# Kernel optimization log

Hardware: AMD Instinct MI355X
Metric: run time of the kernel (lower is better)

## Reference

```python
import jax, jax.numpy as jnp
import numpy as np

EPS = 1e-08


def setup_inputs() -> dict:
    key = jax.random.key(0)
    k1, k2, k3, k4 = jax.random.split(key, 4)
    b, c, h, hw = 16, 512, 32, 32
    out_ch, kk, w_dim = 512, 3, 512
    fan_in = c * kk * kk
    return {
        "x": jax.random.normal(k1, (b, c, h, hw), dtype=jnp.float32),
        "w": jax.random.normal(k2, (b, w_dim), dtype=jnp.float32),
        "weight": jax.random.normal(k3, (out_ch, c, kk, kk), dtype=jnp.float32) / np.sqrt(fan_in),
        "affine_w": jax.random.normal(k4, (c, w_dim), dtype=jnp.float32) * 0.01,
        "affine_b": jnp.ones((c,), dtype=jnp.float32),
    }


def _modconv(x, w, weight, affine_w, affine_b, demod=True):
    b, c, h, hw = x.shape
    kk = weight.shape[-1]
    # style affine: (b, in_ch)
    style = w @ affine_w.T + affine_b
    # per-sample modulated weights: (b, out_ch, in_ch, k, k)
    wgt = weight[None] * style[:, None, :, None, None]
    if demod:
        d = jax.lax.rsqrt(jnp.sum(wgt ** 2, axis=(2, 3, 4)) + EPS)  # (b, out_ch)
        wgt = wgt * d[:, :, None, None, None]

    def conv_one(xi, wi):
        # xi: (c, h, w), wi: (out_ch, c, k, k)
        return jax.lax.conv_general_dilated(
            xi[None], wi, window_strides=(1, 1), padding="SAME",
            dimension_numbers=("NCHW", "OIHW", "NCHW"))[0]

    return jax.vmap(conv_one)(x, wgt)  # (b, out_ch, h, w)


def reference(x, w, weight, affine_w, affine_b):
    return _modconv(x, w, weight, affine_w, affine_b, demod=True)
```

## Files before the change

kernel.cpp:

```cpp
#include <hip/hip_runtime.h>


typedef __attribute__((ext_vector_type(8))) short bfx8;
typedef __attribute__((ext_vector_type(4))) float f32x4;
typedef __attribute__((ext_vector_type(4))) unsigned short us4;
typedef __attribute__((ext_vector_type(8))) unsigned short us8;

__device__ __forceinline__ unsigned short f2bf(float f) {
    unsigned int u = __builtin_bit_cast(unsigned int, f);
    u += 0x7FFFu + ((u >> 16) & 1u);
    return (unsigned short)(u >> 16);
}

__device__ __forceinline__ void gload_lds16(const void* g, void* l) {
    __builtin_amdgcn_global_load_lds(
        (const __attribute__((address_space(1))) unsigned int*)g,
        (__attribute__((address_space(3))) unsigned int*)l,
        16, 0, 0);
}

__device__ __forceinline__ float wave_sum(float v) {
    #pragma unroll
    for (int m = 1; m < 64; m <<= 1) v += __shfl_xor(v, m, 64);
    return v;
}

__device__ __forceinline__ int shift_of(int t) {
    const int tap = t >> 3, q = t & 7;
    const int ky = tap / 3, kx = tap - ky * 3;
    return (ky * 34 + kx) * 512 + q * 64;
}


__global__ void style_kernel(const float* __restrict__ w,
                             const float* __restrict__ affine_w,
                             const float* __restrict__ affine_b,
                             float* __restrict__ style) {
    const int out = blockIdx.x * 4 + (threadIdx.x >> 6);
    const int lane = threadIdx.x & 63;
    const int b = out >> 9, c = out & 511;
    const float4 a0 = *(const float4*)(affine_w + (size_t)c * 512 + lane * 8);
    const float4 a1 = *(const float4*)(affine_w + (size_t)c * 512 + lane * 8 + 4);
    const float4 w0 = *(const float4*)(w + (size_t)b * 512 + lane * 8);
    const float4 w1 = *(const float4*)(w + (size_t)b * 512 + lane * 8 + 4);
    float acc = a0.x * w0.x + a0.y * w0.y + a0.z * w0.z + a0.w * w0.w
              + a1.x * w1.x + a1.y * w1.y + a1.z * w1.z + a1.w * w1.w;
    acc = wave_sum(acc);
    if (lane == 0) style[out] = acc + affine_b[c];
}

__global__ void w2wbf_kernel(const float* __restrict__ weight,
                             float* __restrict__ W2,
                             unsigned short* __restrict__ wbf) {
    const int idx = blockIdx.x * 256 + threadIdx.x;
    const int oc = idx >> 9, c = idx & 511;
    const int q = c >> 6, c_local = c & 63;
    const int s = c_local >> 3, j = c_local & 7;
    const int pos = ((s ^ (oc & 7)) << 3) | j;
    const float* p = weight + (size_t)idx * 9;
    float ss = 0.f;
    #pragma unroll
    for (int t = 0; t < 9; ++t) {
        const float v = p[t];
        ss += v * v;
        wbf[((size_t)(t * 8 + q) * 512 + oc) * 64 + pos] = f2bf(v);
    }
    W2[idx] = ss;
}

__global__ void d_kernel(const float* __restrict__ style,
                         const float* __restrict__ W2,
                         float* __restrict__ dcoef) {
    const int out = blockIdx.x * 4 + (threadIdx.x >> 6);
    const int lane = threadIdx.x & 63;
    const int b = out >> 9, o = out & 511;
    const float4 s0 = *(const float4*)(style + (size_t)b * 512 + lane * 8);
    const float4 s1 = *(const float4*)(style + (size_t)b * 512 + lane * 8 + 4);
    const float4 v0 = *(const float4*)(W2 + (size_t)o * 512 + lane * 8);
    const float4 v1 = *(const float4*)(W2 + (size_t)o * 512 + lane * 8 + 4);
    float acc = s0.x * s0.x * v0.x + s0.y * s0.y * v0.y
              + s0.z * s0.z * v0.z + s0.w * s0.w * v0.w
              + s1.x * s1.x * v1.x + s1.y * s1.y * v1.y
              + s1.z * s1.z * v1.z + s1.w * s1.w * v1.w;
    acc = wave_sum(acc);
    if (lane == 0) dcoef[out] = rsqrtf(acc + 1e-8f);
}

__global__ void border_kernel(unsigned short* __restrict__ xs) {
    const int idx = blockIdx.x * 256 + threadIdx.x;
    const int b = idx / (132 * 128);
    const int r_ = idx - b * (132 * 128);
    const int cell = r_ >> 7, t = r_ & 127;
    int rr, cc;
    if (cell < 34)      { rr = 0;  cc = cell; }
    else if (cell < 68) { rr = 33; cc = cell - 34; }
    else { const int jj = cell - 68; rr = 1 + (jj >> 1); cc = (jj & 1) ? 33 : 0; }
    us4 z = (us4){0, 0, 0, 0};
    *(us4*)(xs + (((size_t)b * 34 + rr) * 34 + cc) * 512 + t * 4) = z;
}

__global__ void xspad_kernel(const float* __restrict__ x,
                             const float* __restrict__ style,
                             unsigned short* __restrict__ xs) {
    __shared__ __align__(16) unsigned short tile[128][36];
    const int b = blockIdx.z, h = blockIdx.y, c0 = blockIdx.x * 128;
    const int tid = threadIdx.x;
    #pragma unroll
    for (int it = 0; it < 4; ++it) {
        const int e = it * 256 + tid;
        const int ch = e >> 3, w4 = e & 7;
        const float4 v = *(const float4*)(x + (((size_t)b * 512 + c0 + ch) * 32 + h) * 32 + w4 * 4);
        const float sv = style[b * 512 + c0 + ch];
        us4 o;
        o.x = f2bf(v.x * sv); o.y = f2bf(v.y * sv);
        o.z = f2bf(v.z * sv); o.w = f2bf(v.w * sv);
        *(us4*)&tile[ch][w4 * 4] = o;
    }
    __syncthreads();
    #pragma unroll
    for (int it = 0; it < 2; ++it) {
        const int e = it * 256 + tid;
        const int cq = e & 15, w_ = e >> 4;
        us8 o;
        #pragma unroll
        for (int i = 0; i < 8; ++i) o[i] = tile[cq * 8 + i][w_];
        *(us8*)(xs + (((size_t)b * 34 + (h + 1)) * 34 + (w_ + 1)) * 512 + c0 + cq * 8) = o;
    }
}

#define LDS_RD(off) (*(const bfx8*)(lds + (off)))
#define MFMA(a, bb, c) __builtin_amdgcn_mfma_f32_16x16x32_bf16((a), (bb), (c), 0, 0, 0)

__global__ __launch_bounds__(512, 2) void conv_kernel(
    const unsigned short* __restrict__ wbf,
    const unsigned short* __restrict__ xs,
    const float* __restrict__ dcoef,
    float* __restrict__ out) {
    __shared__ __align__(16) char lds[147456];

    const int id = blockIdx.x;
    const int b = id >> 4;
    const int oc0 = ((id >> 2) & 3) << 7;
    const int n0  = (id & 3) << 8;

    const int tid = threadIdx.x;
    const int lane = tid & 63;
    const int wv = tid >> 6;
    const int wr = wv >> 2, wc = wv & 3;
    const int l7 = lane & 7, l15 = lane & 15;

    const int swz0 = ((lane >> 4) ^ l7) << 4;
    const int swz1 = (((lane >> 4) + 4) ^ l7) << 4;
    const int arow = (wr * 64 + l15) * 128;
    const int brow = 16384 + (wc * 64 + l15) * 128;

    const int lsub = lane >> 3;
    const int sx = l7 ^ lsub;
    const int ra0 = wv * 16 + lsub, ra1 = ra0 + 8;
    const int aoff0 = (oc0 + ra0) * 64 + l7 * 8;
    const int aoff1 = (oc0 + ra1) * 64 + l7 * 8;
    const int adst0 = (wv * 2) * 1024, adst1 = adst0 + 1024;
    size_t bbase[4]; int bdst[4];
    const size_t xsb = (size_t)b * (34 * 34 * 512);
    #pragma unroll
    for (int i = 0; i < 4; ++i) {
        const int p = wv * 32 + i * 8 + lsub;
        const int n = n0 + p;
        bbase[i] = xsb + ((size_t)(n >> 5) * 34 + (n & 31)) * 512 + sx * 8;
        bdst[i] = 16384 + (wv * 4 + i) * 1024;
    }

#define STAGE_A(tt, bo) do { \
        const unsigned short* wsrc_ = wbf + (size_t)(tt) * 32768; \
        gload_lds16(wsrc_ + aoff0, lds + (bo) + adst0); \
        gload_lds16(wsrc_ + aoff1, lds + (bo) + adst1); } while (0)
#define STAGE_B01(sh, bo) do { \
        gload_lds16(xs + bbase[0] + (sh), lds + (bo) + bdst[0]); \
        gload_lds16(xs + bbase[1] + (sh), lds + (bo) + bdst[1]); } while (0)
#define STAGE_B23(sh, bo) do { \
        gload_lds16(xs + bbase[2] + (sh), lds + (bo) + bdst[2]); \
        gload_lds16(xs + bbase[3] + (sh), lds + (bo) + bdst[3]); } while (0)
#define BARRIER() __builtin_amdgcn_s_barrier()
#define LGKM0() asm volatile("s_waitcnt lgkmcnt(0)" ::: "memory")

    f32x4 acc[4][4];
    #pragma unroll
    for (int i = 0; i < 4; ++i)
        #pragma unroll
        for (int j = 0; j < 4; ++j) acc[i][j] = (f32x4){0.f, 0.f, 0.f, 0.f};

    STAGE_A(0, 0);      STAGE_B01(0, 0);       STAGE_B23(0, 0);
    STAGE_A(1, 49152);  STAGE_B01(64, 49152);  STAGE_B23(64, 49152);
    asm volatile("s_waitcnt vmcnt(6)" ::: "memory");
    BARRIER();

    int co = 0;
    for (int t = 0; t < 72; ++t) {
        int so = co + 98304; if (so >= 147456) so -= 147456;
        const bool pf = (t < 70);
        const int sh2 = pf ? shift_of(t + 2) : 0;

        bfx8 a0[4], a1[4], b0, b1, b2, b3;

        #pragma unroll
        for (int mi = 0; mi < 4; ++mi) a0[mi] = LDS_RD(co + arow + mi * 2048 + swz0);
        b0 = LDS_RD(co + brow + 0 * 2048 + swz0);
        b1 = LDS_RD(co + brow + 1 * 2048 + swz0);
        if (pf) STAGE_A(t + 2, so);
        BARRIER(); LGKM0();
        __builtin_amdgcn_s_setprio(1);
        #pragma unroll
        for (int mi = 0; mi < 4; ++mi) acc[mi][0] = MFMA(a0[mi], b0, acc[mi][0]);
        #pragma unroll
        for (int mi = 0; mi < 4; ++mi) acc[mi][1] = MFMA(a0[mi], b1, acc[mi][1]);
        __builtin_amdgcn_s_setprio(0);
        BARRIER();

        b2 = LDS_RD(co + brow + 2 * 2048 + swz0);
        b3 = LDS_RD(co + brow + 3 * 2048 + swz0);
        if (pf) STAGE_B01(sh2, so);
        BARRIER(); LGKM0();
        __builtin_amdgcn_s_setprio(1);
        #pragma unroll
        for (int mi = 0; mi < 4; ++mi) acc[mi][2] = MFMA(a0[mi], b2, acc[mi][2]);
        #pragma unroll
        for (int mi = 0; mi < 4; ++mi) acc[mi][3] = MFMA(a0[mi], b3, acc[mi][3]);
        __builtin_amdgcn_s_setprio(0);
        BARRIER();

        #pragma unroll
        for (int mi = 0; mi < 4; ++mi) a1[mi] = LDS_RD(co + arow + mi * 2048 + swz1);
        b0 = LDS_RD(co + brow + 0 * 2048 + swz1);
        b1 = LDS_RD(co + brow + 1 * 2048 + swz1);
        if (pf) STAGE_B23(sh2, so);
        BARRIER(); LGKM0();
        __builtin_amdgcn_s_setprio(1);
        #pragma unroll
        for (int mi = 0; mi < 4; ++mi) acc[mi][0] = MFMA(a1[mi], b0, acc[mi][0]);
        #pragma unroll
        for (int mi = 0; mi < 4; ++mi) acc[mi][1] = MFMA(a1[mi], b1, acc[mi][1]);
        __builtin_amdgcn_s_setprio(0);
        BARRIER();

        b2 = LDS_RD(co + brow + 2 * 2048 + swz1);
        b3 = LDS_RD(co + brow + 3 * 2048 + swz1);
        BARRIER(); LGKM0();
        __builtin_amdgcn_s_setprio(1);
        #pragma unroll
        for (int mi = 0; mi < 4; ++mi) acc[mi][2] = MFMA(a1[mi], b2, acc[mi][2]);
        #pragma unroll
        for (int mi = 0; mi < 4; ++mi) acc[mi][3] = MFMA(a1[mi], b3, acc[mi][3]);
        __builtin_amdgcn_s_setprio(0);
        if (t < 70) { asm volatile("s_waitcnt vmcnt(6)" ::: "memory"); }
        else        { asm volatile("s_waitcnt vmcnt(0)" ::: "memory"); }
        BARRIER();

        co += 49152; if (co >= 147456) co -= 147456;
    }

    const int r4 = (lane >> 4) * 4;
    #pragma unroll
    for (int mi = 0; mi < 4; ++mi) {
        #pragma unroll
        for (int rr = 0; rr < 4; ++rr) {
            const int ocr = oc0 + wr * 64 + mi * 16 + r4 + rr;
            const float dv = dcoef[b * 512 + ocr];
            float* orow = out + ((size_t)b * 512 + ocr) * 1024 + n0 + wc * 64 + l15;
            #pragma unroll
            for (int ni = 0; ni < 4; ++ni)
                orow[ni * 16] = acc[mi][ni][rr] * dv;
        }
    }
}

extern "C" void kernel_launch(void* const* d_in, const int* in_sizes, int n_in,
                              void* d_out, int out_size, void* d_ws, size_t ws_size,
                              hipStream_t stream) {
    const float* x        = (const float*)d_in[0];
    const float* w        = (const float*)d_in[1];
    const float* weight   = (const float*)d_in[2];
    const float* affine_w = (const float*)d_in[3];
    const float* affine_b = (const float*)d_in[4];
    float* out = (float*)d_out;

    char* ws = (char*)d_ws;
    float*          style = (float*)(ws + 0);
    float*          W2    = (float*)(ws + 0x8000);
    float*          dcoef = (float*)(ws + 0x108000);
    unsigned short* wbf   = (unsigned short*)(ws + 0x110000);
    unsigned short* xs    = (unsigned short*)(ws + 0x590000);

    style_kernel<<<2048, 256, 0, stream>>>(w, affine_w, affine_b, style);
    w2wbf_kernel<<<1024, 256, 0, stream>>>(weight, W2, wbf);
    d_kernel<<<2048, 256, 0, stream>>>(style, W2, dcoef);
    border_kernel<<<1056, 256, 0, stream>>>(xs);
    xspad_kernel<<<dim3(4, 32, 16), 256, 0, stream>>>(x, style, xs);
    conv_kernel<<<256, 512, 0, stream>>>(wbf, xs, dcoef, out);
}
```

Measured before the change: 106.1 us.

## Merge MFMA phases into two per k-step and remap block IDs across XCDs

Cuts the main loop's four LDS-read/MFMA phases per iteration down to two, each loading all four B fragments and issuing 16 MFMAs. This halves the barrier count per k-step and issues the A and B01 prefetch stages together. It also remaps block IDs so that consecutive blocks land on the same XCD, grouping blocks of the same batch for better L2 reuse. The cost is higher register pressure from holding more fragments at once, and less interleaving of LDS reads with MFMAs.

```diff
diff --git a/kernel.cpp b/kernel.cpp
--- a/kernel.cpp
+++ b/kernel.cpp
@@ -139,9 +139,10 @@
     __shared__ __align__(16) char lds[147456];
 
     const int id = blockIdx.x;
-    const int b = id >> 4;
-    const int oc0 = ((id >> 2) & 3) << 7;
-    const int n0  = (id & 3) << 8;
+    const int wid = (id & 7) * 32 + (id >> 3);
+    const int b = wid >> 4;
+    const int oc0 = ((wid >> 2) & 3) << 7;
+    const int n0  = (wid & 3) << 8;
 
     const int tid = threadIdx.x;
     const int lane = tid & 63;
@@ -200,56 +201,35 @@
         const bool pf = (t < 70);
         const int sh2 = pf ? shift_of(t + 2) : 0;
 
-        bfx8 a0[4], a1[4], b0, b1, b2, b3;
-
-        #pragma unroll
-        for (int mi = 0; mi < 4; ++mi) a0[mi] = LDS_RD(co + arow + mi * 2048 + swz0);
-        b0 = LDS_RD(co + brow + 0 * 2048 + swz0);
-        b1 = LDS_RD(co + brow + 1 * 2048 + swz0);
-        if (pf) STAGE_A(t + 2, so);
+        bfx8 af[4], bx[4];
+
+        #pragma unroll
+        for (int mi = 0; mi < 4; ++mi) af[mi] = LDS_RD(co + arow + mi * 2048 + swz0);
+        #pragma unroll
+        for (int ni = 0; ni < 4; ++ni) bx[ni] = LDS_RD(co + brow + ni * 2048 + swz0);
+        if (pf) { STAGE_A(t + 2, so); STAGE_B01(sh2, so); }
         BARRIER(); LGKM0();
         __builtin_amdgcn_s_setprio(1);
         #pragma unroll
-        for (int mi = 0; mi < 4; ++mi) acc[mi][0] = MFMA(a0[mi], b0, acc[mi][0]);
-        #pragma unroll
-        for (int mi = 0; mi < 4; ++mi) acc[mi][1] = MFMA(a0[mi], b1, acc[mi][1]);
+        for (int ni = 0; ni < 4; ++ni)
+            #pragma unroll
+            for (int mi = 0; mi < 4; ++mi)
+                acc[mi][ni] = MFMA(af[mi], bx[ni], acc[mi][ni]);
         __builtin_amdgcn_s_setprio(0);
         BARRIER();
 
-        b2 = LDS_RD(co + brow + 2 * 2048 + swz0);
-        b3 = LDS_RD(co + brow + 3 * 2048 + swz0);
-        if (pf) STAGE_B01(sh2, so);
-        BARRIER(); LGKM0();
-        __builtin_amdgcn_s_setprio(1);
-        #pragma unroll
-        for (int mi = 0; mi < 4; ++mi) acc[mi][2] = MFMA(a0[mi], b2, acc[mi][2]);
-        #pragma unroll
-        for (int mi = 0; mi < 4; ++mi) acc[mi][3] = MFMA(a0[mi], b3, acc[mi][3]);
-        __builtin_amdgcn_s_setprio(0);
-        BARRIER();
-
-        #pragma unroll
-        for (int mi = 0; mi < 4; ++mi) a1[mi] = LDS_RD(co + arow + mi * 2048 + swz1);
-        b0 = LDS_RD(co + brow + 0 * 2048 + swz1);
-        b1 = LDS_RD(co + brow + 1 * 2048 + swz1);
+        #pragma unroll
+        for (int mi = 0; mi < 4; ++mi) af[mi] = LDS_RD(co + arow + mi * 2048 + swz1);
+        #pragma unroll
+        for (int ni = 0; ni < 4; ++ni) bx[ni] = LDS_RD(co + brow + ni * 2048 + swz1);
         if (pf) STAGE_B23(sh2, so);
         BARRIER(); LGKM0();
         __builtin_amdgcn_s_setprio(1);
         #pragma unroll
-        for (int mi = 0; mi < 4; ++mi) acc[mi][0] = MFMA(a1[mi], b0, acc[mi][0]);
-        #pragma unroll
-        for (int mi = 0; mi < 4; ++mi) acc[mi][1] = MFMA(a1[mi], b1, acc[mi][1]);
-        __builtin_amdgcn_s_setprio(0);
-        BARRIER();
-
-        b2 = LDS_RD(co + brow + 2 * 2048 + swz1);
-        b3 = LDS_RD(co + brow + 3 * 2048 + swz1);
-        BARRIER(); LGKM0();
-        __builtin_amdgcn_s_setprio(1);
-        #pragma unroll
-        for (int mi = 0; mi < 4; ++mi) acc[mi][2] = MFMA(a1[mi], b2, acc[mi][2]);
-        #pragma unroll
-        for (int mi = 0; mi < 4; ++mi) acc[mi][3] = MFMA(a1[mi], b3, acc[mi][3]);
+        for (int ni = 0; ni < 4; ++ni)
+            #pragma unroll
+            for (int mi = 0; mi < 4; ++mi)
+                acc[mi][ni] = MFMA(af[mi], bx[ni], acc[mi][ni]);
         __builtin_amdgcn_s_setprio(0);
         if (t < 70) { asm volatile("s_waitcnt vmcnt(6)" ::: "memory"); }
         else        { asm volatile("s_waitcnt vmcnt(0)" ::: "memory"); }
```

Measured after the change: 105.0 us. About the same (-1.0%).
